# Performance work log

Measured on AMD Instinct MI355X. Metric: run time of the kernel, lower is better.

The kernel has to match this reference:

```python
import jax, jax.numpy as jnp
import numpy as np

N = 50000      # nodes
E = 500000     # edges
IN = 128       # in_channels
HID = 64       # hidden_channels
OUT = 128      # out_channels
H = 4          # heads
NEG_SLOPE = 0.2


def _glorot(key, shape):
    fan_in, fan_out = shape[0], shape[-1]
    lim = np.sqrt(6.0 / (fan_in + fan_out))
    return jax.random.uniform(key, shape, jnp.float32, -lim, lim)


def setup_inputs() -> dict:
    key = jax.random.key(0)
    ks = jax.random.split(key, 12)
    return {
        "x": jax.random.normal(ks[0], (N, IN), jnp.float32),
        "edge_index": jax.random.randint(ks[1], (2, E), 0, N, jnp.int64),
        "edge_weight": jax.random.uniform(ks[2], (E,), jnp.float32),
        # layer 1: IN -> H*HID
        "W1": _glorot(ks[3], (IN, H * HID)),
        "b1": jnp.zeros((H * HID,), jnp.float32),
        "att1": _glorot(ks[4], (H, HID)),
        # layer 2: HID -> H*HID  (update() means over heads -> HID features)
        "W2": _glorot(ks[5], (HID, H * HID)),
        "b2": jnp.zeros((H * HID,), jnp.float32),
        "att2": _glorot(ks[6], (H, HID)),
        # layer 3: HID -> H*OUT
        "W3": _glorot(ks[7], (HID, H * OUT)),
        "b3": jnp.zeros((H * OUT,), jnp.float32),
        "att3": _glorot(ks[8], (H, OUT)),
    }


def _gat_layer(x, W, b, att, src, dst, edge_weight, out_dim):
    # lin + reshape to [N, H, D]
    h = (x @ W + b).reshape(-1, H, out_dim)
    xj = h[src]                                   # gather source feats [E,H,D]
    alpha = jnp.sum(xj * att[None], axis=-1)      # per-edge att score [E,H]
    alpha = jax.nn.leaky_relu(alpha, NEG_SLOPE)
    alpha = alpha * edge_weight[:, None]
    alpha = jax.nn.softmax(alpha, axis=1)         # softmax over HEADS (dim=1, as in source)
    msg = xj * alpha[:, :, None]                  # [E,H,D]
    aggr = jax.ops.segment_sum(msg, dst, num_segments=N)  # scatter-add [N,H,D]
    return aggr.mean(axis=1)                      # update(): mean over heads -> [N,D]


def reference(x, edge_index, edge_weight, W1, b1, att1, W2, b2, att2, W3, b3, att3):
    src, dst = edge_index[0], edge_index[1]
    h = _gat_layer(x, W1, b1, att1, src, dst, edge_weight, HID)
    h = jax.nn.relu(h)
    h = _gat_layer(h, W2, b2, att2, src, dst, edge_weight, HID)
    h = jax.nn.relu(h)
    return _gat_layer(h, W3, b3, att3, src, dst, edge_weight, OUT)
```

## Files before the change

### kernel.cpp

```cpp
#include <hip/hip_runtime.h>
#include <hip/hip_bf16.h>

#define NHEAD 4
#define NEG 0.2f

typedef __bf16 bf16x8 __attribute__((ext_vector_type(8)));
typedef __bf16 bf16x4 __attribute__((ext_vector_type(4)));
typedef float f32x4 __attribute__((ext_vector_type(4)));

__device__ __forceinline__ float blo(unsigned u) { return __uint_as_float(u << 16); }
__device__ __forceinline__ float bhi(unsigned u) { return __uint_as_float(u & 0xffff0000u); }
__device__ __forceinline__ unsigned short fbits(float f) {
    __bf16 h = (__bf16)f;
    return *(unsigned short*)&h;
}


__global__ __launch_bounds__(256) void hist_k(const int* __restrict__ dst,
                                              int* __restrict__ deg, int E) {
    int e = blockIdx.x * 256 + threadIdx.x;
    if (e < E) atomicAdd(&deg[dst[e]], 1);
}

__global__ __launch_bounds__(256) void partial_k(const int* __restrict__ deg,
                                                 int* __restrict__ bsum, int n) {
    int t = threadIdx.x;
    int base = blockIdx.x * 2048 + t * 8;
    int s = 0;
#pragma unroll
    for (int i = 0; i < 8; ++i) {
        int idx = base + i;
        if (idx < n) s += deg[idx];
    }
#pragma unroll
    for (int off = 32; off; off >>= 1) s += __shfl_down(s, off, 64);
    __shared__ int ws[4];
    if ((t & 63) == 0) ws[t >> 6] = s;
    __syncthreads();
    if (t == 0) bsum[blockIdx.x] = ws[0] + ws[1] + ws[2] + ws[3];
}

__global__ __launch_bounds__(256) void bscan_k(const int* __restrict__ bsum,
                                               int* __restrict__ boff, int nb) {
    __shared__ int sh[256];
    int t = threadIdx.x;
    int v = (t < nb) ? bsum[t] : 0;
    sh[t] = v;
    __syncthreads();
    for (int off = 1; off < 256; off <<= 1) {
        int u = (t >= off) ? sh[t - off] : 0;
        __syncthreads();
        sh[t] += u;
        __syncthreads();
    }
    if (t < nb) boff[t] = sh[t] - v;
}

__global__ __launch_bounds__(256) void rescan_k(const int* __restrict__ deg,
                                                const int* __restrict__ boff,
                                                int* __restrict__ rowptr,
                                                int* __restrict__ fill,
                                                int n, int total) {
    __shared__ int ts[256];
    int t = threadIdx.x;
    int base = blockIdx.x * 2048 + t * 8;
    int v[8];
    int s = 0;
#pragma unroll
    for (int i = 0; i < 8; ++i) {
        int idx = base + i;
        v[i] = (idx < n) ? deg[idx] : 0;
        s += v[i];
    }
    ts[t] = s;
    __syncthreads();
    for (int off = 1; off < 256; off <<= 1) {
        int u = (t >= off) ? ts[t - off] : 0;
        __syncthreads();
        ts[t] += u;
        __syncthreads();
    }
    int run = boff[blockIdx.x] + ts[t] - s;
#pragma unroll
    for (int i = 0; i < 8; ++i) {
        int idx = base + i;
        if (idx < n) {
            rowptr[idx] = run;
            fill[idx] = run;
            run += v[i];
        }
    }
    if (blockIdx.x == 0 && t == 0) rowptr[n] = total;
}

__global__ __launch_bounds__(256) void scatter_k(const int* __restrict__ src,
                                                 const int* __restrict__ dst,
                                                 const float* __restrict__ ew,
                                                 int* __restrict__ fill,
                                                 int* __restrict__ srcs,
                                                 float* __restrict__ wsrt, int E) {
    int e = blockIdx.x * 256 + threadIdx.x;
    if (e < E) {
        int d = dst[e];
        int p = atomicAdd(&fill[d], 1);
        srcs[p] = src[e];
        wsrt[p] = ew[e];
    }
}


__global__ __launch_bounds__(256) void prep_k(const float* __restrict__ W1, const float* __restrict__ att1, const float* __restrict__ b1,
                                              const float* __restrict__ W2, const float* __restrict__ att2, const float* __restrict__ b2,
                                              const float* __restrict__ W3, const float* __restrict__ att3, const float* __restrict__ b3,
                                              float* __restrict__ v1, float* __restrict__ v2, float* __restrict__ v3,
                                              float* __restrict__ c1, float* __restrict__ c2, float* __restrict__ c3) {
    int tid = blockIdx.x * 256 + threadIdx.x;
    if (tid < 512) {
        int h = tid >> 7, k = tid & 127;
        float p = 0.f;
        for (int d = 0; d < 64; ++d) p += W1[k * 256 + h * 64 + d] * att1[h * 64 + d];
        v1[h * 128 + k] = p;
    } else if (tid < 768) {
        int t = tid - 512, h = t >> 6, k = t & 63;
        float p = 0.f;
        for (int d = 0; d < 64; ++d) p += W2[k * 256 + h * 64 + d] * att2[h * 64 + d];
        v2[h * 64 + k] = p;
    } else if (tid < 1024) {
        int t = tid - 768, h = t >> 6, k = t & 63;
        float p = 0.f;
        for (int d = 0; d < 128; ++d) p += W3[k * 512 + h * 128 + d] * att3[h * 128 + d];
        v3[h * 64 + k] = p;
    } else if (tid < 1028) {
        int h = tid - 1024;
        float p = 0.f;
        for (int d = 0; d < 64; ++d) p += b1[h * 64 + d] * att1[h * 64 + d];
        c1[h] = p;
    } else if (tid < 1032) {
        int h = tid - 1028;
        float p = 0.f;
        for (int d = 0; d < 64; ++d) p += b2[h * 64 + d] * att2[h * 64 + d];
        c2[h] = p;
    } else if (tid < 1036) {
        int h = tid - 1032;
        float p = 0.f;
        for (int d = 0; d < 128; ++d) p += b3[h * 128 + d] * att3[h * 128 + d];
        c3[h] = p;
    }
}


__global__ __launch_bounds__(256) void wpack3_k(const float* __restrict__ W1,
                                                const float* __restrict__ W2,
                                                const float* __restrict__ W3,
                                                unsigned short* __restrict__ Ws1,
                                                unsigned short* __restrict__ Ws2,
                                                unsigned short* __restrict__ Ws3) {
    int tid = blockIdx.x * 256 + threadIdx.x;
    if (tid < 32768) {
        int d = tid >> 9, r = tid & 511, h = r >> 7, k = r & 127;
        Ws1[tid] = fbits(W1[k * 256 + h * 64 + d]);
    } else if (tid < 49152) {
        int t = tid - 32768;
        int d = t >> 8, r = t & 255, h = r >> 6, k = r & 63;
        Ws2[t] = fbits(W2[k * 256 + h * 64 + d]);
    } else if (tid < 81920) {
        int t = tid - 49152;
        int d = t >> 8, r = t & 255, h = r >> 6, k = r & 63;
        Ws3[t] = fbits(W3[k * 512 + h * 128 + d]);
    }
}


__global__ __launch_bounds__(256) void xpack_score_k(const float* __restrict__ x,
                                                     const float* __restrict__ v1,
                                                     const float* __restrict__ c1,
                                                     unsigned* __restrict__ xb,
                                                     float* __restrict__ s, int n) {
    int gt = blockIdx.x * 256 + threadIdx.x;
    int node = gt >> 6, lane = gt & 63;
    if (node >= n) return;
    float2 xv = ((const float2*)(x + (size_t)node * 128))[lane];
    xb[(size_t)node * 64 + lane] = (unsigned)fbits(xv.x) | ((unsigned)fbits(xv.y) << 16);
    int d0 = 2 * lane;
    float p0 = xv.x * v1[0 * 128 + d0] + xv.y * v1[0 * 128 + d0 + 1];
    float p1 = xv.x * v1[1 * 128 + d0] + xv.y * v1[1 * 128 + d0 + 1];
    float p2 = xv.x * v1[2 * 128 + d0] + xv.y * v1[2 * 128 + d0 + 1];
    float p3 = xv.x * v1[3 * 128 + d0] + xv.y * v1[3 * 128 + d0 + 1];
#pragma unroll
    for (int off = 32; off; off >>= 1) {
        p0 += __shfl_xor(p0, off, 64);
        p1 += __shfl_xor(p1, off, 64);
        p2 += __shfl_xor(p2, off, 64);
        p3 += __shfl_xor(p3, off, 64);
    }
    if (lane == 0)
        *(float4*)&s[(size_t)node * 4] = make_float4(p0 + c1[0], p1 + c1[1], p2 + c1[2], p3 + c1[3]);
}


__global__ __launch_bounds__(256) void alpha_k(const int* __restrict__ srcs,
                                               const float* __restrict__ wsrt,
                                               const float* __restrict__ s,
                                               float* __restrict__ alpha, int E) {
    int e = blockIdx.x * 256 + threadIdx.x;
    if (e >= E) return;
    int sn = srcs[e];
    float w = wsrt[e];
    float4 sv = *(const float4*)&s[(size_t)sn * NHEAD];
    float a0 = (sv.x > 0.f ? sv.x : NEG * sv.x) * w;
    float a1 = (sv.y > 0.f ? sv.y : NEG * sv.y) * w;
    float a2 = (sv.z > 0.f ? sv.z : NEG * sv.z) * w;
    float a3 = (sv.w > 0.f ? sv.w : NEG * sv.w) * w;
    float m = fmaxf(fmaxf(a0, a1), fmaxf(a2, a3));
    float e0 = __expf(a0 - m), e1 = __expf(a1 - m);
    float e2 = __expf(a2 - m), e3 = __expf(a3 - m);
    float inv = 0.25f / (e0 + e1 + e2 + e3);
    *(float4*)&alpha[(size_t)e * 4] = make_float4(e0 * inv, e1 * inv, e2 * inv, e3 * inv);
}


template <int K, int D, bool LAST>
__global__ __launch_bounds__(256, 4) void fused_k(const int* __restrict__ rowptr,
                                                  const int* __restrict__ srcs,
                                                  const float* __restrict__ alpha,
                                                  const unsigned* __restrict__ xb,
                                                  const unsigned short* __restrict__ Ws,
                                                  const float* __restrict__ bias,
                                                  const float* __restrict__ vnext,
                                                  const float* __restrict__ cnext,
                                                  unsigned short* __restrict__ aout,
                                                  float* __restrict__ fout,
                                                  float* __restrict__ snext,
                                                  int n) {
    constexpr int HK = 4 * K;
    constexpr int KS = HK / 32;
    constexpr int NC = D / 16;
    constexpr int CW = NC / 4;
    constexpr int DW = K / 32;

    __shared__ __bf16 g[16 * HK];
    __shared__ float4 A_lds[16];
    __shared__ float4 sc_lds[4][16];

    int t = threadIdx.x;
    int r0 = blockIdx.x * 16;
    int n4 = t >> 4, sl = t & 15;
    int node = r0 + n4;

    float acc[4][2 * DW];
#pragma unroll
    for (int h = 0; h < 4; ++h)
#pragma unroll
        for (int j = 0; j < 2 * DW; ++j) acc[h][j] = 0.f;
    float4 aA = make_float4(0.f, 0.f, 0.f, 0.f);

    auto load_u = [&](int sn, unsigned* u) {
        if constexpr (DW == 4) {
            uint4 ta = ((const uint4*)xb)[(size_t)sn * 16 + sl];
            u[0] = ta.x; u[1] = ta.y; u[2] = ta.z; u[3] = ta.w;
        } else {
            uint2 ta = ((const uint2*)xb)[(size_t)sn * 16 + sl];
            u[0] = ta.x; u[1] = ta.y;
        }
    };
    auto accum = [&](float4 al, const unsigned* u) {
#pragma unroll
        for (int j = 0; j < DW; ++j) {
            float x0 = blo(u[j]), x1 = bhi(u[j]);
            acc[0][2 * j] += al.x * x0; acc[0][2 * j + 1] += al.x * x1;
            acc[1][2 * j] += al.y * x0; acc[1][2 * j + 1] += al.y * x1;
            acc[2][2 * j] += al.z * x0; acc[2][2 * j + 1] += al.z * x1;
            acc[3][2 * j] += al.w * x0; acc[3][2 * j + 1] += al.w * x1;
        }
        aA.x += al.x; aA.y += al.y; aA.z += al.z; aA.w += al.w;
    };

    if (node < n) {
        int beg = rowptr[node], end = rowptr[node + 1];
        int e = beg;
        for (; e + 3 < end; e += 4) {
            int sn0 = srcs[e], sn1 = srcs[e + 1], sn2 = srcs[e + 2], sn3 = srcs[e + 3];
            unsigned u0[DW], u1[DW], u2[DW], u3[DW];
            load_u(sn0, u0); load_u(sn1, u1); load_u(sn2, u2); load_u(sn3, u3);
            float4 al0 = *(const float4*)&alpha[(size_t)e * 4];
            float4 al1 = *(const float4*)&alpha[(size_t)(e + 1) * 4];
            float4 al2 = *(const float4*)&alpha[(size_t)(e + 2) * 4];
            float4 al3 = *(const float4*)&alpha[(size_t)(e + 3) * 4];
            accum(al0, u0); accum(al1, u1); accum(al2, u2); accum(al3, u3);
        }
        for (; e < end; ++e) {
            int sn = srcs[e];
            unsigned u[DW];
            load_u(sn, u);
            float4 al = *(const float4*)&alpha[(size_t)e * 4];
            accum(al, u);
        }
    }

    int wid = t >> 6, lane = t & 63;
    int lrow = lane & 15, gq = lane >> 4;

    auto write_part = [&](bool lo) {
        char* gb = (char*)g + (size_t)n4 * (HK * 2);
        int sw = (n4 & 7) << 4;
#pragma unroll
        for (int h = 0; h < 4; ++h) {
            if constexpr (DW == 4) {
                bf16x8 v;
#pragma unroll
                for (int j = 0; j < 8; ++j) {
                    float a = acc[h][j];
                    __bf16 hi = (__bf16)a;
                    v[j] = lo ? (__bf16)(a - (float)hi) : hi;
                }
                int bo = (h * K + sl * 8) * 2;
                *(bf16x8*)(gb + (bo ^ sw)) = v;
            } else {
                bf16x4 v;
#pragma unroll
                for (int j = 0; j < 4; ++j) {
                    float a = acc[h][j];
                    __bf16 hi = (__bf16)a;
                    v[j] = lo ? (__bf16)(a - (float)hi) : hi;
                }
                int bo = (h * K + sl * 4) * 2;
                *(bf16x4*)(gb + (bo ^ sw)) = v;
            }
        }
    };

    f32x4 acc2[CW];
#pragma unroll
    for (int cw = 0; cw < CW; ++cw)
#pragma unroll
        for (int r = 0; r < 4; ++r) acc2[cw][r] = 0.f;

    const __bf16* wsp = (const __bf16*)Ws;
    const char* gr = (const char*)g + (size_t)lrow * (HK * 2);
    int swr = (lrow & 7) << 4;

    auto mfma_pass = [&]() {
#pragma unroll
        for (int ks = 0; ks < KS; ++ks) {
            int bo = ks * 64 + gq * 16;
            bf16x8 fr = *(const bf16x8*)(gr + (bo ^ swr));
#pragma unroll
            for (int cw = 0; cw < CW; ++cw) {
                int c = wid * CW + cw;
                bf16x8 bfr = *(const bf16x8*)(wsp + (size_t)(c * 16 + lrow) * HK + ks * 32 + gq * 8);
                acc2[cw] = __builtin_amdgcn_mfma_f32_16x16x32_bf16(fr, bfr, acc2[cw], 0, 0, 0);
            }
        }
    };

    write_part(false);
    if (sl == 0) A_lds[n4] = aA;
    __syncthreads();
    mfma_pass();
    __syncthreads();
    write_part(true);
    __syncthreads();
    mfma_pass();

    float4 Ar[4];
#pragma unroll
    for (int r = 0; r < 4; ++r) Ar[r] = A_lds[gq * 4 + r];

    float sc[4][4];
#pragma unroll
    for (int h = 0; h < 4; ++h)
#pragma unroll
        for (int r = 0; r < 4; ++r) sc[h][r] = 0.f;

#pragma unroll
    for (int cw = 0; cw < CW; ++cw) {
        int col = (wid * CW + cw) * 16 + lrow;
        float bb0 = bias[0 * D + col], bb1 = bias[1 * D + col];
        float bb2 = bias[2 * D + col], bb3 = bias[3 * D + col];
        float vv0 = 0.f, vv1 = 0.f, vv2 = 0.f, vv3 = 0.f;
        if constexpr (!LAST) {
            vv0 = vnext[0 * D + col]; vv1 = vnext[1 * D + col];
            vv2 = vnext[2 * D + col]; vv3 = vnext[3 * D + col];
        }
#pragma unroll
        for (int r = 0; r < 4; ++r) {
            float val = acc2[cw][r] + Ar[r].x * bb0 + Ar[r].y * bb1 + Ar[r].z * bb2 + Ar[r].w * bb3;
            int row = r0 + gq * 4 + r;
            if constexpr (LAST) {
                if (row < n) fout[(size_t)row * D + col] = val;
            } else {
                val = fmaxf(val, 0.f);
                if (row < n) aout[(size_t)row * D + col] = fbits(val);
                sc[0][r] += val * vv0;
                sc[1][r] += val * vv1;
                sc[2][r] += val * vv2;
                sc[3][r] += val * vv3;
            }
        }
    }

    if constexpr (!LAST) {
#pragma unroll
        for (int m = 1; m < 16; m <<= 1) {
#pragma unroll
            for (int h = 0; h < 4; ++h)
#pragma unroll
                for (int r = 0; r < 4; ++r) sc[h][r] += __shfl_xor(sc[h][r], m, 64);
        }
        if (lrow < 4) {
            int r = lrow;
            sc_lds[wid][gq * 4 + r] = make_float4(sc[0][r], sc[1][r], sc[2][r], sc[3][r]);
        }
        __syncthreads();
        if (t < 16) {
            int row = r0 + t;
            if (row < n) {
                float4 s0 = sc_lds[0][t], s1 = sc_lds[1][t];
                float4 s2 = sc_lds[2][t], s3 = sc_lds[3][t];
                *(float4*)&snext[(size_t)row * 4] =
                    make_float4(s0.x + s1.x + s2.x + s3.x + cnext[0],
                                s0.y + s1.y + s2.y + s3.y + cnext[1],
                                s0.z + s1.z + s2.z + s3.z + cnext[2],
                                s0.w + s1.w + s2.w + s3.w + cnext[3]);
            }
        }
    }
}


extern "C" void kernel_launch(void* const* d_in, const int* in_sizes, int n_in,
                              void* d_out, int out_size, void* d_ws, size_t ws_size,
                              hipStream_t stream) {
    const float* x    = (const float*)d_in[0];
    const int*   ei   = (const int*)d_in[1];
    const float* ew   = (const float*)d_in[2];
    const float* W1   = (const float*)d_in[3];
    const float* b1   = (const float*)d_in[4];
    const float* att1 = (const float*)d_in[5];
    const float* W2   = (const float*)d_in[6];
    const float* b2   = (const float*)d_in[7];
    const float* att2 = (const float*)d_in[8];
    const float* W3   = (const float*)d_in[9];
    const float* b3   = (const float*)d_in[10];
    const float* att3 = (const float*)d_in[11];

    const int N = in_sizes[0] / 128;
    const int E = in_sizes[2];
    const int* src = ei;
    const int* dst = ei + E;

    char* wp = (char*)d_ws;
    auto alloc = [&](size_t bytes) -> void* {
        void* p = (void*)wp;
        wp += (bytes + 511) & ~(size_t)511;
        return p;
    };
    int*   deg    = (int*)alloc((size_t)N * 4);
    int*   rowptr = (int*)alloc((size_t)(N + 1) * 4);
    int*   fill   = (int*)alloc((size_t)N * 4);
    int*   bsum   = (int*)alloc(256 * 4);
    int*   boff   = (int*)alloc(256 * 4);
    int*   srcs   = (int*)alloc((size_t)E * 4);
    float* wsrt   = (float*)alloc((size_t)E * 4);
    unsigned* xb  = (unsigned*)alloc((size_t)N * 64 * 4);
    float* s      = (float*)alloc((size_t)N * 4 * 4);
    float* s2     = (float*)alloc((size_t)N * 4 * 4);
    float* alpha  = (float*)alloc((size_t)E * 4 * 4);
    unsigned short* a1 = (unsigned short*)alloc((size_t)N * 64 * 2);
    unsigned short* a2 = (unsigned short*)alloc((size_t)N * 64 * 2);
    float* v1 = (float*)alloc(512 * 4);
    float* v2 = (float*)alloc(256 * 4);
    float* v3 = (float*)alloc(256 * 4);
    float* c1 = (float*)alloc(16);
    float* c2 = (float*)alloc(16);
    float* c3 = (float*)alloc(16);
    unsigned short* Ws1 = (unsigned short*)alloc(32768 * 2);
    unsigned short* Ws2 = (unsigned short*)alloc(16384 * 2);
    unsigned short* Ws3 = (unsigned short*)alloc(32768 * 2);

    wpack3_k<<<320, 256, 0, stream>>>(W1, W2, W3, Ws1, Ws2, Ws3);
    prep_k<<<5, 256, 0, stream>>>(W1, att1, b1, W2, att2, b2, W3, att3, b3,
                                  v1, v2, v3, c1, c2, c3);
    int gx = (N * 64 + 255) / 256;
    xpack_score_k<<<gx, 256, 0, stream>>>(x, v1, c1, xb, s, N);

    hipMemsetAsync(deg, 0, (size_t)N * 4, stream);
    int ge = (E + 255) / 256;
    int nb = (N + 2047) / 2048;
    hist_k<<<ge, 256, 0, stream>>>(dst, deg, E);
    partial_k<<<nb, 256, 0, stream>>>(deg, bsum, N);
    bscan_k<<<1, 256, 0, stream>>>(bsum, boff, nb);
    rescan_k<<<nb, 256, 0, stream>>>(deg, boff, rowptr, fill, N, E);
    scatter_k<<<ge, 256, 0, stream>>>(src, dst, ew, fill, srcs, wsrt, E);

    int gf = (N + 15) / 16;

    alpha_k<<<ge, 256, 0, stream>>>(srcs, wsrt, s, alpha, E);
    fused_k<128, 64, false><<<gf, 256, 0, stream>>>(rowptr, srcs, alpha, xb, Ws1, b1,
                                                    v2, c2, a1, nullptr, s2, N);

    alpha_k<<<ge, 256, 0, stream>>>(srcs, wsrt, s2, alpha, E);
    fused_k<64, 64, false><<<gf, 256, 0, stream>>>(rowptr, srcs, alpha, (const unsigned*)a1,
                                                   Ws2, b2, v3, c3, a2, nullptr, s, N);

    alpha_k<<<ge, 256, 0, stream>>>(srcs, wsrt, s, alpha, E);
    fused_k<64, 128, true><<<gf, 256, 0, stream>>>(rowptr, srcs, alpha, (const unsigned*)a2,
                                                   Ws3, b3, nullptr, nullptr, nullptr,
                                                   (float*)d_out, nullptr, N);
}
```

Baseline: 291.3 us.

## Split fused GAT gather over K halves to cut registers and raise occupancy

The fused aggregate-plus-GEMM kernel now processes the feature dimension in 64-wide chunks, looping the edge gather once per chunk with a fixed 4x4 accumulator. Hi and lo bf16 parts go to separate shared buffers and are consumed in one MFMA pass per chunk, and launch bounds rise to six blocks per CU. This is meant to shrink register and LDS use per block to raise occupancy for the latency-bound gather. The cost is that edge indices and alpha are re-read once per chunk for K=128, with extra syncs.

```diff
diff --git a/kernel.cpp b/kernel.cpp
--- a/kernel.cpp
+++ b/kernel.cpp
@@ -220,7 +220,7 @@
 
 
 template <int K, int D, bool LAST>
-__global__ __launch_bounds__(256, 4) void fused_k(const int* __restrict__ rowptr,
+__global__ __launch_bounds__(256, 6) void fused_k(const int* __restrict__ rowptr,
                                                   const int* __restrict__ srcs,
                                                   const float* __restrict__ alpha,
                                                   const unsigned* __restrict__ xb,
@@ -233,12 +233,13 @@
                                                   float* __restrict__ snext,
                                                   int n) {
     constexpr int HK = 4 * K;
-    constexpr int KS = HK / 32;
+    constexpr int KH = K / 64;
     constexpr int NC = D / 16;
     constexpr int CW = NC / 4;
-    constexpr int DW = K / 32;
-
-    __shared__ __bf16 g[16 * HK];
+    constexpr int RU2 = K / 4;
+
+    __shared__ __bf16 gsth[16 * 256];
+    __shared__ __bf16 gstl[16 * 256];
     __shared__ float4 A_lds[16];
     __shared__ float4 sc_lds[4][16];
 
@@ -246,121 +247,100 @@
     int r0 = blockIdx.x * 16;
     int n4 = t >> 4, sl = t & 15;
     int node = r0 + n4;
-
-    float acc[4][2 * DW];
-#pragma unroll
-    for (int h = 0; h < 4; ++h)
-#pragma unroll
-        for (int j = 0; j < 2 * DW; ++j) acc[h][j] = 0.f;
-    float4 aA = make_float4(0.f, 0.f, 0.f, 0.f);
-
-    auto load_u = [&](int sn, unsigned* u) {
-        if constexpr (DW == 4) {
-            uint4 ta = ((const uint4*)xb)[(size_t)sn * 16 + sl];
-            u[0] = ta.x; u[1] = ta.y; u[2] = ta.z; u[3] = ta.w;
-        } else {
-            uint2 ta = ((const uint2*)xb)[(size_t)sn * 16 + sl];
-            u[0] = ta.x; u[1] = ta.y;
-        }
-    };
-    auto accum = [&](float4 al, const unsigned* u) {
-#pragma unroll
-        for (int j = 0; j < DW; ++j) {
-            float x0 = blo(u[j]), x1 = bhi(u[j]);
-            acc[0][2 * j] += al.x * x0; acc[0][2 * j + 1] += al.x * x1;
-            acc[1][2 * j] += al.y * x0; acc[1][2 * j + 1] += al.y * x1;
-            acc[2][2 * j] += al.z * x0; acc[2][2 * j + 1] += al.z * x1;
-            acc[3][2 * j] += al.w * x0; acc[3][2 * j + 1] += al.w * x1;
-        }
-        aA.x += al.x; aA.y += al.y; aA.z += al.z; aA.w += al.w;
-    };
-
-    if (node < n) {
-        int beg = rowptr[node], end = rowptr[node + 1];
+    int wid = t >> 6, lane = t & 63;
+    int lrow = lane & 15, gq = lane >> 4;
+
+    int beg = 0, end = 0;
+    if (node < n) { beg = rowptr[node]; end = rowptr[node + 1]; }
+
+    f32x4 acc2[CW];
+#pragma unroll
+    for (int cw = 0; cw < CW; ++cw)
+#pragma unroll
+        for (int r = 0; r < 4; ++r) acc2[cw][r] = 0.f;
+
+    const uint2* xr = (const uint2*)xb;
+    const __bf16* wsp = (const __bf16*)Ws;
+    const char* ghr = (const char*)gsth + (size_t)lrow * 512;
+    const char* glr = (const char*)gstl + (size_t)lrow * 512;
+    int swr = (lrow & 7) << 4;
+
+    for (int kh = 0; kh < KH; ++kh) {
+        float acc[4][4];
+#pragma unroll
+        for (int h = 0; h < 4; ++h)
+#pragma unroll
+            for (int j = 0; j < 4; ++j) acc[h][j] = 0.f;
+        float4 aA = make_float4(0.f, 0.f, 0.f, 0.f);
+
+        auto accum1 = [&](float4 al, uint2 u) {
+            float x0 = blo(u.x), x1 = bhi(u.x), x2 = blo(u.y), x3 = bhi(u.y);
+            acc[0][0] += al.x * x0; acc[0][1] += al.x * x1; acc[0][2] += al.x * x2; acc[0][3] += al.x * x3;
+            acc[1][0] += al.y * x0; acc[1][1] += al.y * x1; acc[1][2] += al.y * x2; acc[1][3] += al.y * x3;
+            acc[2][0] += al.z * x0; acc[2][1] += al.z * x1; acc[2][2] += al.z * x2; acc[2][3] += al.z * x3;
+            acc[3][0] += al.w * x0; acc[3][1] += al.w * x1; acc[3][2] += al.w * x2; acc[3][3] += al.w * x3;
+            aA.x += al.x; aA.y += al.y; aA.z += al.z; aA.w += al.w;
+        };
+
         int e = beg;
         for (; e + 3 < end; e += 4) {
             int sn0 = srcs[e], sn1 = srcs[e + 1], sn2 = srcs[e + 2], sn3 = srcs[e + 3];
-            unsigned u0[DW], u1[DW], u2[DW], u3[DW];
-            load_u(sn0, u0); load_u(sn1, u1); load_u(sn2, u2); load_u(sn3, u3);
+            uint2 u0 = xr[(size_t)sn0 * RU2 + kh * 16 + sl];
+            uint2 u1 = xr[(size_t)sn1 * RU2 + kh * 16 + sl];
+            uint2 u2 = xr[(size_t)sn2 * RU2 + kh * 16 + sl];
+            uint2 u3 = xr[(size_t)sn3 * RU2 + kh * 16 + sl];
             float4 al0 = *(const float4*)&alpha[(size_t)e * 4];
             float4 al1 = *(const float4*)&alpha[(size_t)(e + 1) * 4];
             float4 al2 = *(const float4*)&alpha[(size_t)(e + 2) * 4];
             float4 al3 = *(const float4*)&alpha[(size_t)(e + 3) * 4];
-            accum(al0, u0); accum(al1, u1); accum(al2, u2); accum(al3, u3);
+            accum1(al0, u0); accum1(al1, u1); accum1(al2, u2); accum1(al3, u3);
         }
         for (; e < end; ++e) {
-            int sn = srcs[e];
-            unsigned u[DW];
-            load_u(sn, u);
+            uint2 u = xr[(size_t)srcs[e] * RU2 + kh * 16 + sl];
             float4 al = *(const float4*)&alpha[(size_t)e * 4];
-            accum(al, u);
-        }
-    }
-
-    int wid = t >> 6, lane = t & 63;
-    int lrow = lane & 15, gq = lane >> 4;
-
-    auto write_part = [&](bool lo) {
-        char* gb = (char*)g + (size_t)n4 * (HK * 2);
-        int sw = (n4 & 7) << 4;
-#pragma unroll
-        for (int h = 0; h < 4; ++h) {
-            if constexpr (DW == 4) {
-                bf16x8 v;
-#pragma unroll
-                for (int j = 0; j < 8; ++j) {
-                    float a = acc[h][j];
-                    __bf16 hi = (__bf16)a;
-                    v[j] = lo ? (__bf16)(a - (float)hi) : hi;
-                }
-                int bo = (h * K + sl * 8) * 2;
-                *(bf16x8*)(gb + (bo ^ sw)) = v;
-            } else {
-                bf16x4 v;
+            accum1(al, u);
+        }
+
+        if (kh) __syncthreads();
+
+        {
+            char* ghb = (char*)gsth + (size_t)n4 * 512;
+            char* glb = (char*)gstl + (size_t)n4 * 512;
+            int sw = (n4 & 7) << 4;
+#pragma unroll
+            for (int h = 0; h < 4; ++h) {
+                bf16x4 vh, vl;
 #pragma unroll
                 for (int j = 0; j < 4; ++j) {
                     float a = acc[h][j];
                     __bf16 hi = (__bf16)a;
-                    v[j] = lo ? (__bf16)(a - (float)hi) : hi;
+                    vh[j] = hi;
+                    vl[j] = (__bf16)(a - (float)hi);
                 }
-                int bo = (h * K + sl * 4) * 2;
-                *(bf16x4*)(gb + (bo ^ sw)) = v;
+                int bo = h * 128 + sl * 8;
+                *(bf16x4*)(ghb + (bo ^ sw)) = vh;
+                *(bf16x4*)(glb + (bo ^ sw)) = vl;
             }
-        }
-    };
-
-    f32x4 acc2[CW];
-#pragma unroll
-    for (int cw = 0; cw < CW; ++cw)
-#pragma unroll
-        for (int r = 0; r < 4; ++r) acc2[cw][r] = 0.f;
-
-    const __bf16* wsp = (const __bf16*)Ws;
-    const char* gr = (const char*)g + (size_t)lrow * (HK * 2);
-    int swr = (lrow & 7) << 4;
-
-    auto mfma_pass = [&]() {
-#pragma unroll
-        for (int ks = 0; ks < KS; ++ks) {
-            int bo = ks * 64 + gq * 16;
-            bf16x8 fr = *(const bf16x8*)(gr + (bo ^ swr));
+            if (kh == 0 && sl == 0) A_lds[n4] = aA;
+        }
+        __syncthreads();
+
+#pragma unroll
+        for (int ksl = 0; ksl < 8; ++ksl) {
+            int h = ksl >> 1, kk = ksl & 1;
+            int bo = h * 128 + kk * 64 + gq * 16;
+            bf16x8 fh = *(const bf16x8*)(ghr + (bo ^ swr));
+            bf16x8 fl = *(const bf16x8*)(glr + (bo ^ swr));
 #pragma unroll
             for (int cw = 0; cw < CW; ++cw) {
                 int c = wid * CW + cw;
-                bf16x8 bfr = *(const bf16x8*)(wsp + (size_t)(c * 16 + lrow) * HK + ks * 32 + gq * 8);
-                acc2[cw] = __builtin_amdgcn_mfma_f32_16x16x32_bf16(fr, bfr, acc2[cw], 0, 0, 0);
+                const __bf16* bp = wsp + (size_t)(c * 16 + lrow) * HK + h * K + kh * 64 + kk * 32 + gq * 8;
+                bf16x8 bfr = *(const bf16x8*)bp;
+                acc2[cw] = __builtin_amdgcn_mfma_f32_16x16x32_bf16(fh, bfr, acc2[cw], 0, 0, 0);
+                acc2[cw] = __builtin_amdgcn_mfma_f32_16x16x32_bf16(fl, bfr, acc2[cw], 0, 0, 0);
             }
         }
-    };
-
-    write_part(false);
-    if (sl == 0) A_lds[n4] = aA;
-    __syncthreads();
-    mfma_pass();
-    __syncthreads();
-    write_part(true);
-    __syncthreads();
-    mfma_pass();
+    }
 
     float4 Ar[4];
 #pragma unroll
```

New measurement: 262.4 us. 9.9% less time.
